# Performance work log

Measured on AMD Instinct MI355X. Metric: run time of the kernel, lower is better.

Reference implementation:

```python
import jax, jax.numpy as jnp
import numpy as np
from jax import lax


def conv1x1(x, w, b):
    # x [B,Ci,H,W], w [Co,Ci], b [Co]
    return jnp.einsum('oi,bihw->bohw', w, x) + b[None, :, None, None]


def dil_conv_relu(x, w, b):
    # 3x3 conv, dilation 2, padding 2 (make_layers with dilation=True), then ReLU
    y = lax.conv_general_dilated(x, w, (1, 1), [(2, 2), (2, 2)], rhs_dilation=(2, 2),
                                 dimension_numbers=('NCHW', 'OIHW', 'NCHW'))
    return jax.nn.relu(y + b[None, :, None, None])


def conv1d_relu(x, w, b):
    # x [n,c,L], w [o,i,9], padding 4 -> same length; conv + ReLU (nn.Sequential(Conv2d, ReLU))
    y = lax.conv_general_dilated(x, w, (1,), [(4, 4)], dimension_numbers=('NCH', 'OIH', 'NCH'))
    return jax.nn.relu(y + b[None, :, None])


def dulr_pass(slices, w, b):
    # slices [L,n,c,m]; out[0]=slices[0]; out[i]=convrelu(out[i-1]) + slices[i]
    def step(carry, s):
        new = conv1d_relu(carry, w, b) + s
        return new, new
    _, rest = lax.scan(step, slices[0], slices[1:])
    return jnp.concatenate([slices[:1], rest], axis=0)


def conv_du(x, w, b):
    # down pass then up pass over rows (kernel (1,9) -> 1D conv along width)
    rows = jnp.moveaxis(x, 2, 0)            # [h,n,c,w]
    rows = dulr_pass(rows, w, b)
    rows = dulr_pass(rows[::-1], w, b)[::-1]
    return jnp.moveaxis(rows, 0, 2)


def conv_lr(x, w, b):
    # left-right then right-left over columns (kernel (9,1) -> 1D conv along height)
    cols = jnp.moveaxis(x, 3, 0)            # [w,n,c,h]
    cols = dulr_pass(cols, w, b)
    cols = dulr_pass(cols[::-1], w, b)[::-1]
    return jnp.moveaxis(cols, 0, 3)


def setup_inputs() -> dict:
    key = jax.random.key(0)
    ks = jax.random.split(key, 24)
    B, H, W = 4, 64, 64
    std = 0.01
    f32 = jnp.float32
    d = {}
    d['in_data'] = jax.random.normal(ks[0], (B, 1025, H, W), f32)
    d['wA'] = jax.random.normal(ks[1], (128, 1024), f32) * std
    d['bA'] = jax.random.normal(ks[2], (128,), f32) * std
    d['wB'] = jax.random.normal(ks[3], (128, 1024), f32) * std
    d['bB'] = jax.random.normal(ks[4], (128,), f32) * std
    d['wC'] = jax.random.normal(ks[5], (1024, 1024), f32) * std
    d['bC'] = jax.random.normal(ks[6], (1024,), f32) * std
    d['gamma'] = jnp.array(0.1, f32)
    chans = [(512, 1024), (512, 512), (512, 512), (256, 512), (128, 256), (64, 128)]
    for i, (co, ci) in enumerate(chans):
        d[f'bw{i+1}'] = jax.random.normal(ks[7 + 2 * i], (co, ci, 3, 3), f32) * std
        d[f'bb{i+1}'] = jax.random.normal(ks[8 + 2 * i], (co,), f32) * std
    d['du_w'] = jax.random.normal(ks[19], (64, 64, 9), f32) * std
    d['du_b'] = jax.random.normal(ks[20], (64,), f32) * std
    d['lr_w'] = jax.random.normal(ks[21], (64, 64, 9), f32) * std
    d['lr_b'] = jax.random.normal(ks[22], (64,), f32) * std
    d['ow'] = jax.random.normal(ks[23], (1, 64), f32) * std
    d['ob'] = jnp.zeros((1,), f32)
    return d


def reference(in_data, wA, bA, wB, bB, wC, bC, gamma,
              bw1, bb1, bw2, bb2, bw3, bb3, bw4, bb4, bw5, bb5, bw6, bb6,
              du_w, du_b, lr_w, lr_b, ow, ob):
    x = in_data[:, :1024]                   # [B,1024,H,W]
    f = in_data[:, 1024:1025]               # [B,1,H,W]
    B, C, H, W = x.shape
    N = H * W
    # appearance_A(x) -> query [B,128,N]
    q = conv1x1(x, wA, bA).reshape(B, 128, N)
    # f1024 = f broadcast to 1024 channels; flow_B(f1024) (1x1 conv) == f * sum_i wB[:,i] + bB
    k = (f * wB.sum(axis=1)[None, :, None, None] + bB[None, :, None, None]).reshape(B, 128, N)
    energy = jnp.einsum('bcn,bcm->bnm', q, k)           # [B,N,N] = q^T k
    att = jax.nn.softmax(energy, axis=-1)
    v = conv1x1(x, wC, bC).reshape(B, C, N)             # appearance_C
    out = jnp.einsum('bcj,bij->bci', v, att).reshape(B, C, H, W)  # bmm(v, att^T)
    x = gamma * out + x
    for w_, b_ in ((bw1, bb1), (bw2, bb2), (bw3, bb3), (bw4, bb4), (bw5, bb5), (bw6, bb6)):
        x = dil_conv_relu(x, w_, b_)
    x = conv_du(x, du_w, du_b)
    x = conv_lr(x, lr_w, lr_b)
    x = jax.nn.relu(conv1x1(x, ow, ob))                 # o_layer
    # F.upsample(scale_factor=8) default nearest
    x = jnp.repeat(jnp.repeat(x, 8, axis=2), 8, axis=3)
    return x
```

## Files before the change

kernel.cpp:

```cpp
#include <hip/hip_runtime.h>


#define NPIX 4096

typedef _Float16 f16;
typedef _Float16 f16x8 __attribute__((ext_vector_type(8)));
typedef _Float16 f16x4 __attribute__((ext_vector_type(4)));
typedef float f32x4 __attribute__((ext_vector_type(4)));

__device__ inline void async16(const void* g, void* l) {
  __builtin_amdgcn_global_load_lds(
      (const __attribute__((address_space(1))) unsigned int*)g,
      (__attribute__((address_space(3))) unsigned int*)l, 16, 0, 0);
}


__global__ void rf_zero(float* __restrict__ z) { z[threadIdx.x] = 0.f; }

__global__ void rf_s(const float* __restrict__ wB, const float* __restrict__ bA,
                     float* __restrict__ s_out, float* __restrict__ c0_out) {
  int c = threadIdx.x;
  const float* row = wB + (size_t)c * 1024;
  float acc = 0.f;
  for (int i = 0; i < 1024; ++i) acc += row[i];
  s_out[c] = acc;
  __shared__ float sh[128];
  sh[c] = acc * bA[c];
  __syncthreads();
  for (int off = 64; off > 0; off >>= 1) {
    if (c < off) sh[c] += sh[c + off];
    __syncthreads();
  }
  if (c == 0) c0_out[0] = sh[0];
}

__global__ void rf_u(const float* __restrict__ wA, const float* __restrict__ s,
                     float* __restrict__ u) {
  int i = blockIdx.x * 256 + threadIdx.x;
  float acc = 0.f;
  for (int c = 0; c < 128; ++c) acc += s[c] * wA[(size_t)c * 1024 + i];
  u[i] = acc;
}

__global__ void rf_fstat(const float* __restrict__ in, float* __restrict__ fstat) {
  int b = blockIdx.x;
  int t = threadIdx.x;
  const float* f = in + ((size_t)b * 1025 + 1024) * NPIX;
  float mx = -1e30f, mn = 1e30f;
  for (int j = t; j < NPIX; j += 256) {
    float v = f[j];
    mx = fmaxf(mx, v);
    mn = fminf(mn, v);
  }
  __shared__ float smx[256], smn[256];
  smx[t] = mx; smn[t] = mn;
  __syncthreads();
  for (int off = 128; off > 0; off >>= 1) {
    if (t < off) {
      smx[t] = fmaxf(smx[t], smx[t + off]);
      smn[t] = fminf(smn[t], smn[t + off]);
    }
    __syncthreads();
  }
  if (t == 0) { fstat[b] = smx[0]; fstat[4 + b] = smn[0]; }
}

__global__ __launch_bounds__(256) void rf_A(const float* __restrict__ in,
                                            const float* __restrict__ u,
                                            const float* __restrict__ c0p,
                                            const float* __restrict__ fst,
                                            float* __restrict__ A, float* __restrict__ M) {
  __shared__ float ul[1024];
  int b = blockIdx.y;
  int n = blockIdx.x * 256 + threadIdx.x;
  for (int s = threadIdx.x; s < 1024; s += 256) ul[s] = u[s];
  __syncthreads();
  const float* xp = in + (size_t)b * 1025 * NPIX + n;
  float acc = c0p[0];
#pragma unroll 8
  for (int i = 0; i < 1024; ++i) acc = fmaf(ul[i], xp[(size_t)i * NPIX], acc);
  A[b * NPIX + n] = acc;
  M[b * NPIX + n] = fmaxf(acc * fst[b], acc * fst[4 + b]);
}

__global__ void rf_Z(const float* __restrict__ in, const float* __restrict__ A,
                     const float* __restrict__ M, float* __restrict__ iZ) {
  int idx = blockIdx.x * 4 + (threadIdx.x >> 6);
  int lane = threadIdx.x & 63;
  int b = idx >> 12;
  const float* f = in + ((size_t)b * 1025 + 1024) * NPIX;
  float a = A[idx], m = M[idx];
  float acc = 0.f;
#pragma unroll 4
  for (int it = 0; it < 64; ++it) acc += __expf(a * f[lane + it * 64] - m);
  for (int off = 32; off > 0; off >>= 1) acc += __shfl_down(acc, off, 64);
  if (lane == 0) iZ[idx] = 1.0f / acc;
}


__global__ void rf_xsplit(const float* __restrict__ in, f16* __restrict__ xh) {
  __shared__ float tl[64][65];
  int nt = blockIdx.x, ct = blockIdx.y, b = blockIdx.z;
  int n0 = nt * 64, c0 = ct * 64;
  int tid = threadIdx.x;
  for (int s = tid; s < 4096; s += 256) {
    int r = s >> 6, c = s & 63;
    tl[r][c] = in[((size_t)b * 1025 + c0 + r) * NPIX + n0 + c];
  }
  __syncthreads();
  for (int s = tid; s < 512; s += 256) {
    int n = s >> 3, g = s & 7;
    f16x8 hb;
#pragma unroll
    for (int q = 0; q < 8; ++q) hb[q] = (f16)(16.f * tl[g * 8 + q][n]);
    size_t o = ((size_t)b * NPIX + n0 + n) * 1024 + c0 + g * 8;
    *(f16x8*)&xh[o] = hb;
  }
}


__global__ void rf_wC1(const float* __restrict__ wC, f16* __restrict__ wh) {
  int base = (blockIdx.x * 256 + threadIdx.x) * 8;
  f16x8 hb;
#pragma unroll
  for (int q = 0; q < 8; ++q) hb[q] = (f16)(256.f * wC[base + q]);
  *(f16x8*)&wh[base] = hb;
}


__global__ __launch_bounds__(256, 2) void rf_vgemmm(
    const f16* __restrict__ wh, const f16* __restrict__ xh,
    const float* __restrict__ bC, f16* __restrict__ vH) {
  __shared__ f16 sA[2][4096], sB[2][4096];
  const int tid = threadIdx.x;
  const int nb = blockIdx.x * 128, cb = blockIdx.y * 128, b = blockIdx.z;
  const int pA = tid & 127;
  const int wv = tid >> 6, lane = tid & 63;
  const int mrow = lane & 15, quad = lane >> 4;
  const int wm = (wv & 1) * 64, wn = (wv >> 1) * 64;
  const size_t abase = (size_t)(cb + pA) * 1024;
  const size_t bbase = ((size_t)b * NPIX + nb + pA) * 1024;
  f32x4 acc[4][4];
#pragma unroll
  for (int i = 0; i < 4; ++i)
#pragma unroll
    for (int j = 0; j < 4; ++j) acc[i][j] = (f32x4){0.f, 0.f, 0.f, 0.f};

  auto stage = [&](int k0, int pb) {
#pragma unroll
    for (int s = 0; s < 2; ++s) {
      const int cc = ((tid + 256 * s) >> 7) & 3;
      const int lb = ((tid & ~63) + 256 * s) * 8;
      async16(wh + abase + k0 + cc * 8, &sA[pb][lb]);
      async16(xh + bbase + k0 + cc * 8, &sB[pb][lb]);
    }
  };
  stage(0, 0);
  int p = 0;
  for (int k0 = 0; k0 < 1024; k0 += 32) {
    __syncthreads();
    if (k0 + 32 < 1024) stage(k0 + 32, p ^ 1);
    f16x8 fa[4], fb[4];
#pragma unroll
    for (int mi = 0; mi < 4; ++mi)
      fa[mi] = *(const f16x8*)&sA[p][(quad * 128 + wm + mi * 16 + mrow) * 8];
#pragma unroll
    for (int ni = 0; ni < 4; ++ni)
      fb[ni] = *(const f16x8*)&sB[p][(quad * 128 + wn + ni * 16 + mrow) * 8];
#pragma unroll
    for (int mi = 0; mi < 4; ++mi)
#pragma unroll
      for (int ni = 0; ni < 4; ++ni)
        acc[mi][ni] = __builtin_amdgcn_mfma_f32_16x16x32_f16(fa[mi], fb[ni], acc[mi][ni], 0, 0, 0);
    p ^= 1;
  }
  const float inv = 1.0f / 4096.0f;
#pragma unroll
  for (int mi = 0; mi < 4; ++mi) {
#pragma unroll
    for (int rg = 0; rg < 4; ++rg) {
      int c = cb + wm + mi * 16 + quad * 4 + rg;
      float bv = bC[c];
#pragma unroll
      for (int ni = 0; ni < 4; ++ni) {
        int j = nb + wn + ni * 16 + mrow;
        vH[((size_t)b * 1024 + c) * NPIX + j] =
            (f16)(16.f * (acc[mi][ni][rg] * inv + bv));
      }
    }
  }
}


__global__ __launch_bounds__(256, 2) void rf_attm(
    const f16* __restrict__ vH,
    const float* __restrict__ Aarr, const float* __restrict__ Marr,
    const float* __restrict__ iZ, const float* __restrict__ in,
    const float* __restrict__ gptr, f16* __restrict__ yH) {
  __shared__ f16 sAh[2][8192];
  __shared__ f16 sPh[2][4096];
  const int tid = threadIdx.x;
  const int ib = blockIdx.x * 128, cb = blockIdx.y * 256, b = blockIdx.z;
  const int wv = tid >> 6, lane = tid & 63;
  const int mrow = lane & 15, quad = lane >> 4;
  const int wm = wv * 64;
  const int ni_ = tid & 127;
  const int kc0 = tid >> 7;
  const float av2 = Aarr[b * NPIX + ib + ni_] * 1.44269504f;
  const float mv2 = Marr[b * NPIX + ib + ni_] * 1.44269504f;
  const float* f = in + ((size_t)b * 1025 + 1024) * NPIX;
  const f16* vrow = vH + ((size_t)b * 1024 + cb + tid) * NPIX;

  f32x4 acc[4][8];
#pragma unroll
  for (int i = 0; i < 4; ++i)
#pragma unroll
    for (int j = 0; j < 8; ++j) acc[i][j] = (f32x4){0.f, 0.f, 0.f, 0.f};

  auto stage = [&](int j0, int pb) {
#pragma unroll
    for (int s = 0; s < 4; ++s)
      async16(vrow + j0 + s * 8, &sAh[pb][(s * 256 + tid) * 8]);
  };
  auto doP = [&](int j0, int pb) {
#pragma unroll
    for (int it = 0; it < 2; ++it) {
      const int kc = kc0 + 2 * it;
      const float4 fa4 = *(const float4*)&f[j0 + kc * 8];
      const float4 fb4 = *(const float4*)&f[j0 + kc * 8 + 4];
      const float fj[8] = {fa4.x, fa4.y, fa4.z, fa4.w, fb4.x, fb4.y, fb4.z, fb4.w};
      f16x8 ph;
#pragma unroll
      for (int q = 0; q < 8; ++q)
        ph[q] = (f16)exp2f(fmaf(av2, fj[q], -mv2));
      *(f16x8*)&sPh[pb][(kc * 128 + ni_) * 8] = ph;
    }
  };

  stage(0, 0);
  doP(0, 0);
  int p = 0;
  for (int k = 0; k < 128; ++k) {
    __syncthreads();
    f16x8 fa[4], fb[8];
#pragma unroll
    for (int mi = 0; mi < 4; ++mi)
      fa[mi] = *(const f16x8*)&sAh[p][(quad * 256 + wm + mi * 16 + mrow) * 8];
#pragma unroll
    for (int ni = 0; ni < 8; ++ni)
      fb[ni] = *(const f16x8*)&sPh[p][(quad * 128 + ni * 16 + mrow) * 8];
    if (k < 127) {
      stage((k + 1) * 32, p ^ 1);
      doP((k + 1) * 32, p ^ 1);
    }
#pragma unroll
    for (int mi = 0; mi < 4; ++mi)
#pragma unroll
      for (int ni = 0; ni < 8; ++ni)
        acc[mi][ni] = __builtin_amdgcn_mfma_f32_16x16x32_f16(fa[mi], fb[ni], acc[mi][ni], 0, 0, 0);
    p ^= 1;
  }

  const float g = gptr[0];
  const float inv16 = 1.0f / 16.0f;
  float zvi[8];
#pragma unroll
  for (int ni = 0; ni < 8; ++ni)
    zvi[ni] = iZ[b * NPIX + ib + ni * 16 + mrow] * inv16;
#pragma unroll
  for (int mi = 0; mi < 4; ++mi) {
    const int cbase = cb + wm + mi * 16 + quad * 4;
#pragma unroll
    for (int ni = 0; ni < 8; ++ni) {
      const int i = ib + ni * 16 + mrow;
      f16x4 hv;
#pragma unroll
      for (int rg = 0; rg < 4; ++rg) {
        float xr = in[((size_t)b * 1025 + cbase + rg) * NPIX + i];
        hv[rg] = (f16)(16.f * (g * (acc[mi][ni][rg] * zvi[ni]) + xr));
      }
      *(f16x4*)&yH[((size_t)b * NPIX + i) * 1024 + cbase] = hv;
    }
  }
}


__global__ void rf_wfragc(const float* __restrict__ w, f16* __restrict__ F,
                          int CI, int CO) {
  int gid = blockIdx.x * 256 + threadIdx.x;
  const int C16 = CO >> 4, KI = CI >> 5;
  const int total = 9 * KI * C16 * 64;
  if (gid >= total) return;
  int lane = gid & 63;
  int rest = gid >> 6;
  int c16 = rest % C16;
  int rest2 = rest / C16;
  int k = rest2 % KI;
  int t = rest2 / KI;
  int co = c16 * 16 + (lane & 15);
  int ci = k * 32 + (lane >> 4) * 8;
  f16x8 hb;
#pragma unroll
  for (int j = 0; j < 8; ++j)
    hb[j] = (f16)(256.0f * w[((size_t)co * CI + ci + j) * 9 + t]);
  *(f16x8*)&F[(size_t)gid * 8] = hb;
}


template <int BM, int BN, bool F32OUT>
__global__ __launch_bounds__(256, 2) void rf_mconv(
    const f16* __restrict__ xh, const f16* __restrict__ F,
    const float* __restrict__ bias, const float* __restrict__ zp,
    f16* __restrict__ oh, float* __restrict__ of, int CI, int CO) {
  constexpr int ROWS = BM / 64;
  constexpr int TPI = 4096 / BM;
  constexpr int HROWS = ROWS + 4;
  constexpr int COLP = 72;
  constexpr int CHUNKS = HROWS * 4 * COLP;
  constexpr int NSTG = (CHUNKS + 255) / 256;
  __shared__ f16 sA[2][NSTG * 2048];
  const int tid = threadIdx.x;
  const int blkpx = blockIdx.x;
  const int cob = blockIdx.y * BN;
  const int b = blkpx / TPI;
  const int h0 = (blkpx - b * TPI) * ROWS;

  const int wv = tid >> 6, lane = tid & 63;
  const int mrow = lane & 15, quad = lane >> 4;
  const int wm = (BN == 128) ? (wv & 1) * 64 : wv * 64;
  const int wn = (BN == 128) ? (wv >> 1) * 64 : 0;
  const int r_out = wm >> 6;
  const int KI = CI >> 5;
  const int C16 = CO >> 4;
  const int cb16 = (cob + wn) >> 4;

  f32x4 acc[4][4];
#pragma unroll
  for (int i = 0; i < 4; ++i)
#pragma unroll
    for (int j = 0; j < 4; ++j) acc[i][j] = (f32x4){0.f, 0.f, 0.f, 0.f};

  const f16* abase[NSTG];
  unsigned vmask = 0;
#pragma unroll
  for (int s = 0; s < NSTG; ++s) {
    int idx = tid + 256 * s;
    int rowks = idx / COLP;
    int col = idx - rowks * COLP;
    int r = rowks >> 2, ks = rowks & 3;
    int srow = h0 + r - 2, scol = col - 2;
    bool ok = (idx < CHUNKS) && ((unsigned)srow < 64u) && ((unsigned)scol < 64u);
    abase[s] = ok ? xh + (((size_t)b * 64 + srow) * 64 + scol) * CI + ks * 8
                  : (const f16*)zp;
    if (ok) vmask |= (1u << s);
  }
  auto stageA = [&](int k, int pb) {
#pragma unroll
    for (int s = 0; s < NSTG; ++s) {
      const f16* sp = abase[s] + (((vmask >> s) & 1u) ? k * 32 : 0);
      async16(sp, &sA[pb][((tid & ~63) + 256 * s) * 8]);
    }
  };

  const f16* Fb = F + ((size_t)cb16 * 64 + lane) * 8;

  stageA(0, 0);
  int p = 0;
  for (int k = 0; k < KI; ++k) {
    __syncthreads();
    if (k + 1 < KI) stageA(k + 1, p ^ 1);
#pragma unroll
    for (int t = 0; t < 9; ++t) {
      const int dh = (t / 3) * 2 - 2, dw = (t - (t / 3) * 3) * 2 - 2;
      f16x8 fb[4];
#pragma unroll
      for (int ni = 0; ni < 4; ++ni)
        fb[ni] = *(const f16x8*)(Fb + ((size_t)(t * KI + k) * C16 + ni) * 512);
      f16x8 fa[4];
#pragma unroll
      for (int mi = 0; mi < 4; ++mi)
        fa[mi] = *(const f16x8*)&sA[p][(((r_out + dh + 2) * 4 + quad) * COLP +
                                       mi * 16 + mrow + dw + 2) * 8];
#pragma unroll
      for (int mi = 0; mi < 4; ++mi)
#pragma unroll
        for (int ni = 0; ni < 4; ++ni)
          acc[mi][ni] = __builtin_amdgcn_mfma_f32_16x16x32_f16(fa[mi], fb[ni], acc[mi][ni], 0, 0, 0);
    }
    p ^= 1;
  }

  const float inv = 1.0f / 4096.0f;
  float bvs[4];
#pragma unroll
  for (int ni = 0; ni < 4; ++ni) bvs[ni] = bias[cob + wn + ni * 16 + mrow];
#pragma unroll
  for (int mi = 0; mi < 4; ++mi) {
#pragma unroll
    for (int rg = 0; rg < 4; ++rg) {
      int px = wm + mi * 16 + quad * 4 + rg;
      int hh = h0 + (px >> 6), wwp = px & 63;
#pragma unroll
      for (int ni = 0; ni < 4; ++ni) {
        int co = cob + wn + ni * 16 + mrow;
        float vv = fmaxf(acc[mi][ni][rg] * inv + bvs[ni], 0.f);
        if (F32OUT) {
          of[(((size_t)b * CO + co) * 64 + hh) * 64 + wwp] = vv;
        } else {
          oh[(((size_t)b * 64 + hh) * 64 + wwp) * CO + co] = (f16)(vv * 16.f);
        }
      }
    }
  }
}


__global__ void rf_wfrag(const float* __restrict__ w, f16* __restrict__ fh) {
  int gid = blockIdx.x * 256 + threadIdx.x;
  if (gid >= 4608) return;
  int lane = gid & 63;
  int rem = gid >> 6;
  int kc = rem & 1;
  int rem2 = rem >> 1;
  int t = rem2 % 9;
  int w4 = rem2 / 9;
  int co = w4 * 16 + (lane & 15);
  int cib = kc * 32 + (lane >> 4) * 8;
  f16x8 hb;
#pragma unroll
  for (int j = 0; j < 8; ++j)
    hb[j] = (f16)(256.f * w[((size_t)co * 64 + cib + j) * 9 + t]);
  *(f16x8*)&fh[(size_t)gid * 8] = hb;
}


__global__ __launch_bounds__(256, 1) void rf_mscan(
    const float* __restrict__ src, float* __restrict__ dst,
    const f16* __restrict__ fh, const float* __restrict__ bias, int dir) {
  __shared__ f16 ch[72 * 64];
  const int b = blockIdx.x;
  const int tid = threadIdx.x;
  const int wave = tid >> 6, lane = tid & 63;
  const int quad = lane >> 4, l15 = lane & 15;

  f16x8 Ah[9][2];
#pragma unroll
  for (int t = 0; t < 9; ++t)
#pragma unroll
    for (int kc = 0; kc < 2; ++kc)
      Ah[t][kc] = *(const f16x8*)&fh[(((wave * 9 + t) * 2 + kc) * 64 + lane) * 8];
  float bvs[4];
#pragma unroll
  for (int r = 0; r < 4; ++r) bvs[r] = bias[wave * 16 + quad * 4 + r];

  for (int s = tid; s < 2304; s += 256) ((unsigned*)ch)[s] = 0u;
  __syncthreads();

  const size_t sbase = (size_t)b * 64 * 4096;
  const int row0 = (dir > 0) ? 0 : 63;
  {
    int pos0 = tid & 63, cig = tid >> 6;
#pragma unroll
    for (int q = 0; q < 16; ++q) {
      int ci = cig * 16 + q;
      float v = src[sbase + (size_t)ci * 4096 + row0 * 64 + pos0];
      dst[sbase + (size_t)ci * 4096 + row0 * 64 + pos0] = v;
      int rowIdx = pos0 + 4;
      ch[rowIdx * 64 + (((ci >> 3) ^ (rowIdx & 7)) << 3) + (ci & 7)] = (f16)v;
    }
  }
  __syncthreads();

  const float inv = 1.0f / 256.0f;
  for (int s = 1; s < 64; ++s) {
    const int row = (dir > 0) ? s : 63 - s;
    float srow[4][4];
#pragma unroll
    for (int nt = 0; nt < 4; ++nt)
#pragma unroll
      for (int r = 0; r < 4; ++r)
        srow[nt][r] = src[sbase + (size_t)(wave * 16 + quad * 4 + r) * 4096 +
                          row * 64 + nt * 16 + l15];
    f32x4 acc[4];
#pragma unroll
    for (int nt = 0; nt < 4; ++nt) acc[nt] = (f32x4){0.f, 0.f, 0.f, 0.f};
#pragma unroll
    for (int t = 0; t < 9; ++t)
#pragma unroll
      for (int kc = 0; kc < 2; ++kc) {
#pragma unroll
        for (int nt = 0; nt < 4; ++nt) {
          int rowIdx = nt * 16 + l15 + t;
          int gr = kc * 4 + quad;
          f16x8 Bh = *(const f16x8*)&ch[rowIdx * 64 + ((gr ^ (rowIdx & 7)) << 3)];
          acc[nt] = __builtin_amdgcn_mfma_f32_16x16x32_f16(Ah[t][kc], Bh, acc[nt], 0, 0, 0);
        }
      }
    __syncthreads();
#pragma unroll
    for (int nt = 0; nt < 4; ++nt) {
      int pos = nt * 16 + l15;
      int rowIdx = pos + 4;
      f16x4 hv;
#pragma unroll
      for (int r = 0; r < 4; ++r) {
        float v = fmaxf(acc[nt][r] * inv + bvs[r], 0.f) + srow[nt][r];
        dst[sbase + (size_t)(wave * 16 + quad * 4 + r) * 4096 + row * 64 + pos] = v;
        hv[r] = (f16)v;
      }
      int ci0 = wave * 16 + quad * 4;
      *(f16x4*)&ch[rowIdx * 64 + (((ci0 >> 3) ^ (rowIdx & 7)) << 3) + (ci0 & 7)] = hv;
    }
    __syncthreads();
  }
}


__global__ void rf_transpose(const float* __restrict__ src, float* __restrict__ dst) {
  int bc = blockIdx.x;
  __shared__ float tl[64][65];
  int tid = threadIdx.x;
  const float* sp = src + (size_t)bc * 4096;
  float* dp = dst + (size_t)bc * 4096;
  for (int s = tid; s < 4096; s += 256) {
    int h = s >> 6, w = s & 63;
    tl[w][h] = sp[s];
  }
  __syncthreads();
  for (int s = tid; s < 4096; s += 256) dp[s] = tl[s >> 6][s & 63];
}


__global__ void rf_final(const float* __restrict__ t, const float* __restrict__ ow,
                         const float* __restrict__ ob, float* __restrict__ out) {
  int b = blockIdx.y;
  int s = blockIdx.x * 256 + threadIdx.x;
  int w = s >> 6, h = s & 63;
  float acc = ob[0];
  for (int c = 0; c < 64; ++c)
    acc += ow[c] * t[(((size_t)b * 64 + c) * 64 + w) * 64 + h];
  acc = fmaxf(acc, 0.f);
  float4 vv = make_float4(acc, acc, acc, acc);
  for (int dy = 0; dy < 8; ++dy) {
    float* dp = out + ((size_t)b * 512 + h * 8 + dy) * 512 + w * 8;
    *(float4*)dp = vv;
    *(float4*)(dp + 4) = vv;
  }
}


extern "C" void kernel_launch(void* const* d_in, const int* in_sizes, int n_in,
                              void* d_out, int out_size, void* d_ws, size_t ws_size,
                              hipStream_t stream) {
  const float* in    = (const float*)d_in[0];
  const float* wA    = (const float*)d_in[1];
  const float* bA    = (const float*)d_in[2];
  const float* wB    = (const float*)d_in[3];
  const float* wC    = (const float*)d_in[5];
  const float* bC    = (const float*)d_in[6];
  const float* gamma = (const float*)d_in[7];
  const float* bw1 = (const float*)d_in[8];  const float* bb1 = (const float*)d_in[9];
  const float* bw2 = (const float*)d_in[10]; const float* bb2 = (const float*)d_in[11];
  const float* bw3 = (const float*)d_in[12]; const float* bb3 = (const float*)d_in[13];
  const float* bw4 = (const float*)d_in[14]; const float* bb4 = (const float*)d_in[15];
  const float* bw5 = (const float*)d_in[16]; const float* bb5 = (const float*)d_in[17];
  const float* bw6 = (const float*)d_in[18]; const float* bb6 = (const float*)d_in[19];
  const float* du_w = (const float*)d_in[20]; const float* du_b = (const float*)d_in[21];
  const float* lr_w = (const float*)d_in[22]; const float* lr_b = (const float*)d_in[23];
  const float* ow   = (const float*)d_in[24]; const float* ob   = (const float*)d_in[25];
  float* out = (float*)d_out;
  float* ws = (float*)d_ws;

  f16* vH  = (f16*)(ws + 0);
  f16* xTh = (f16*)(ws + 4194304);
  f16* wCh = (f16*)(ws + 8388608);
  f16* yH  = (f16*)(ws + 16777216);
  f16* w1h = (f16*)(ws + 0);
  f16* c1H = (f16*)(ws + 2359296);
  f16* w3h = (f16*)(ws + 6553600);
  f16* w2h = (f16*)(ws + 16777216);
  f16* c2H = (f16*)(ws + 17956864);
  f16* w4h = (f16*)(ws + 22151168);
  f16* c4H = (f16*)(ws + 22740992);
  f16* c3H = c1H;
  f16* w5h = (f16*)(ws + 0);
  f16* c5H = (f16*)(ws + 147456);
  f16* w6h = (f16*)(ws + 1196032);
  float* tin = ws + 1232896;
  float* t0  = ws + 2281472;
  float* t1  = ws + 3330048;
  f16* duFh = (f16*)(ws + 4378624);
  f16* lrFh = (f16*)(ws + 4397056);
  float* sm = ws + 33554432;
  float* A_  = sm;
  float* M_  = sm + 16384;
  float* iZ  = sm + 32768;
  float* u_  = sm + 49152;
  float* s_  = sm + 50176;
  float* c0_ = sm + 50304;
  float* fst = sm + 50308;
  float* zp  = sm + 50432;

  rf_zero<<<1, 64, 0, stream>>>(zp);
  rf_s<<<1, 128, 0, stream>>>(wB, bA, s_, c0_);
  rf_u<<<4, 256, 0, stream>>>(wA, s_, u_);
  rf_fstat<<<4, 256, 0, stream>>>(in, fst);
  rf_A<<<dim3(16, 4), 256, 0, stream>>>(in, u_, c0_, fst, A_, M_);
  rf_Z<<<4096, 256, 0, stream>>>(in, A_, M_, iZ);
  rf_xsplit<<<dim3(64, 16, 4), 256, 0, stream>>>(in, xTh);
  rf_wC1<<<512, 256, 0, stream>>>(wC, wCh);
  rf_vgemmm<<<dim3(32, 8, 4), 256, 0, stream>>>(wCh, xTh, bC, vH);
  rf_attm<<<dim3(32, 4, 4), 256, 0, stream>>>(vH, A_, M_, iZ, in, gamma, yH);

  rf_wfragc<<<2304, 256, 0, stream>>>(bw1, w1h, 1024, 512);
  rf_wfragc<<<1152, 256, 0, stream>>>(bw3, w3h, 512, 512);
  rf_mconv<128, 128, false><<<dim3(128, 4), 256, 0, stream>>>(
      yH, w1h, bb1, zp, c1H, nullptr, 1024, 512);
  rf_wfragc<<<1152, 256, 0, stream>>>(bw2, w2h, 512, 512);
  rf_wfragc<<<576, 256, 0, stream>>>(bw4, w4h, 512, 256);
  rf_wfragc<<<144, 256, 0, stream>>>(bw5, w5h, 256, 128);
  rf_wfragc<<<36, 256, 0, stream>>>(bw6, w6h, 128, 64);
  rf_mconv<128, 128, false><<<dim3(128, 4), 256, 0, stream>>>(
      c1H, w2h, bb2, zp, c2H, nullptr, 512, 512);
  rf_mconv<128, 128, false><<<dim3(128, 4), 256, 0, stream>>>(
      c2H, w3h, bb3, zp, c3H, nullptr, 512, 512);
  rf_mconv<128, 128, false><<<dim3(128, 2), 256, 0, stream>>>(
      c3H, w4h, bb4, zp, c4H, nullptr, 512, 256);
  rf_wfrag<<<18, 256, 0, stream>>>(du_w, duFh);
  rf_wfrag<<<18, 256, 0, stream>>>(lr_w, lrFh);
  rf_mconv<128, 128, false><<<dim3(128, 1), 256, 0, stream>>>(
      c4H, w5h, bb5, zp, c5H, nullptr, 256, 128);
  rf_mconv<256, 64, true><<<dim3(64, 1), 256, 0, stream>>>(
      c5H, w6h, bb6, zp, nullptr, tin, 128, 64);

  rf_mscan<<<4, 256, 0, stream>>>(tin, t0, duFh, du_b, +1);
  rf_mscan<<<4, 256, 0, stream>>>(t0, t1, duFh, du_b, -1);
  rf_transpose<<<256, 256, 0, stream>>>(t1, t0);
  rf_mscan<<<4, 256, 0, stream>>>(t0, t1, lrFh, lr_b, +1);
  rf_mscan<<<4, 256, 0, stream>>>(t1, t0, lrFh, lr_b, -1);
  rf_final<<<dim3(16, 4), 256, 0, stream>>>(t0, ow, ob, out);
}
```

Measured before the change: 1.702 ms.

## Triple-buffer V tiles and stage flow row in LDS in attention-apply kernel

The attention-apply kernel now uses a three-stage LDS ring for the V tiles, issuing async loads two iterations ahead, and waits with explicit vmcnt/lgkmcnt counts plus raw barriers instead of __syncthreads. The flow row f for the batch is copied once into LDS so the exp computation reads it from shared memory rather than global memory. The goal is to hide global load latency behind the MFMA work. In exchange LDS use grows by about 32 KB per block, which may reduce occupancy below the two blocks per CU requested by the launch bounds, and the hand-written wait counts must match the number of outstanding loads exactly.

```diff
diff --git a/kernel.cpp b/kernel.cpp
--- a/kernel.cpp
+++ b/kernel.cpp
@@ -197,8 +197,9 @@
     const float* __restrict__ Aarr, const float* __restrict__ Marr,
     const float* __restrict__ iZ, const float* __restrict__ in,
     const float* __restrict__ gptr, f16* __restrict__ yH) {
-  __shared__ f16 sAh[2][8192];
+  __shared__ f16 sAh[3][8192];
   __shared__ f16 sPh[2][4096];
+  __shared__ float fl[4096];
   const int tid = threadIdx.x;
   const int ib = blockIdx.x * 128, cb = blockIdx.y * 256, b = blockIdx.z;
   const int wv = tid >> 6, lane = tid & 63;
@@ -226,8 +227,8 @@
 #pragma unroll
     for (int it = 0; it < 2; ++it) {
       const int kc = kc0 + 2 * it;
-      const float4 fa4 = *(const float4*)&f[j0 + kc * 8];
-      const float4 fb4 = *(const float4*)&f[j0 + kc * 8 + 4];
+      const float4 fa4 = *(const float4*)&fl[j0 + kc * 8];
+      const float4 fb4 = *(const float4*)&fl[j0 + kc * 8 + 4];
       const float fj[8] = {fa4.x, fa4.y, fa4.z, fa4.w, fb4.x, fb4.y, fb4.z, fb4.w};
       f16x8 ph;
 #pragma unroll
@@ -237,28 +238,67 @@
     }
   };
 
+#pragma unroll
+  for (int s = 0; s < 4; ++s)
+    async16(f + (tid + 256 * s) * 4, &fl[((tid & ~63) + 256 * s) * 4]);
   stage(0, 0);
+  asm volatile("s_waitcnt vmcnt(0)" ::: "memory");
+  __builtin_amdgcn_s_barrier();
   doP(0, 0);
-  int p = 0;
-  for (int k = 0; k < 128; ++k) {
-    __syncthreads();
+  stage(32, 1);
+  asm volatile("s_waitcnt lgkmcnt(0)" ::: "memory");
+  __builtin_amdgcn_s_barrier();
+
+  for (int k = 0; k < 126; ++k) {
+    const int pa = k % 3;
+    const int pp = k & 1;
     f16x8 fa[4], fb[8];
 #pragma unroll
     for (int mi = 0; mi < 4; ++mi)
-      fa[mi] = *(const f16x8*)&sAh[p][(quad * 256 + wm + mi * 16 + mrow) * 8];
+      fa[mi] = *(const f16x8*)&sAh[pa][(quad * 256 + wm + mi * 16 + mrow) * 8];
 #pragma unroll
     for (int ni = 0; ni < 8; ++ni)
-      fb[ni] = *(const f16x8*)&sPh[p][(quad * 128 + ni * 16 + mrow) * 8];
-    if (k < 127) {
-      stage((k + 1) * 32, p ^ 1);
-      doP((k + 1) * 32, p ^ 1);
-    }
+      fb[ni] = *(const f16x8*)&sPh[pp][(quad * 128 + ni * 16 + mrow) * 8];
+    stage((k + 2) * 32, (k + 2) % 3);
+    doP((k + 1) * 32, pp ^ 1);
 #pragma unroll
     for (int mi = 0; mi < 4; ++mi)
 #pragma unroll
       for (int ni = 0; ni < 8; ++ni)
         acc[mi][ni] = __builtin_amdgcn_mfma_f32_16x16x32_f16(fa[mi], fb[ni], acc[mi][ni], 0, 0, 0);
-    p ^= 1;
+    asm volatile("s_waitcnt vmcnt(4) lgkmcnt(0)" ::: "memory");
+    __builtin_amdgcn_s_barrier();
+  }
+  {
+    f16x8 fa[4], fb[8];
+#pragma unroll
+    for (int mi = 0; mi < 4; ++mi)
+      fa[mi] = *(const f16x8*)&sAh[0][(quad * 256 + wm + mi * 16 + mrow) * 8];
+#pragma unroll
+    for (int ni = 0; ni < 8; ++ni)
+      fb[ni] = *(const f16x8*)&sPh[0][(quad * 128 + ni * 16 + mrow) * 8];
+    doP(127 * 32, 1);
+#pragma unroll
+    for (int mi = 0; mi < 4; ++mi)
+#pragma unroll
+      for (int ni = 0; ni < 8; ++ni)
+        acc[mi][ni] = __builtin_amdgcn_mfma_f32_16x16x32_f16(fa[mi], fb[ni], acc[mi][ni], 0, 0, 0);
+    asm volatile("s_waitcnt vmcnt(0) lgkmcnt(0)" ::: "memory");
+    __builtin_amdgcn_s_barrier();
+  }
+  {
+    f16x8 fa[4], fb[8];
+#pragma unroll
+    for (int mi = 0; mi < 4; ++mi)
+      fa[mi] = *(const f16x8*)&sAh[1][(quad * 256 + wm + mi * 16 + mrow) * 8];
+#pragma unroll
+    for (int ni = 0; ni < 8; ++ni)
+      fb[ni] = *(const f16x8*)&sPh[1][(quad * 128 + ni * 16 + mrow) * 8];
+#pragma unroll
+    for (int mi = 0; mi < 4; ++mi)
+#pragma unroll
+      for (int ni = 0; ni < 8; ++ni)
+        acc[mi][ni] = __builtin_amdgcn_mfma_f32_16x16x32_f16(fa[mi], fb[ni], acc[mi][ni], 0, 0, 0);
   }
 
   const float g = gptr[0];
```

Measured after the change: 1.683 ms. About the same (-1.2%).
